# Kernel tuning notes

Hardware: AMD Instinct MI355X
Metric: run time of the kernel (lower is better)

## Reference

```python
import jax, jax.numpy as jnp
import numpy as np

N_NODES = 100000
N_EDGES = 1600000
IN_DIM = 128
HID = 128
Z_DIM = 16
NUM_LAYERS = 3


def gcn_conv(x, W, b, src, dst, num_nodes):
    """PyG-style GCNConv with self-loops and symmetric normalization.
    src/dst already include self-loops. x: [N, Fin], W: [Fin, Fout]."""
    xw = x @ W  # [N, Fout]
    deg = jax.ops.segment_sum(jnp.ones(src.shape[0], dtype=x.dtype), dst,
                              num_segments=num_nodes)  # >=1 due to self-loops
    dinv = jax.lax.rsqrt(jnp.maximum(deg, 1.0))
    norm = dinv[src] * dinv[dst]  # [E]
    msg = xw[src] * norm[:, None]  # [E, Fout] gather
    out = jax.ops.segment_sum(msg, dst, num_segments=num_nodes)  # scatter-add
    return out + b


def setup_inputs() -> dict:
    key = jax.random.key(0)
    ks = jax.random.split(key, 10)
    adj = jax.random.randint(ks[0], (2, N_EDGES), 0, N_NODES, dtype=jnp.int32)
    X = jax.random.normal(ks[1], (N_NODES, IN_DIM), dtype=jnp.float32)
    s = 0.05
    fc1_W = jax.random.normal(ks[2], (IN_DIM, 128), dtype=jnp.float32) * s
    fc1_b = jnp.zeros((128,), dtype=jnp.float32)
    fc2_W = jax.random.normal(ks[3], (128, HID), dtype=jnp.float32) * s
    fc2_b = jnp.zeros((HID,), dtype=jnp.float32)
    gcn_W = jax.random.normal(ks[4], (NUM_LAYERS, HID, HID), dtype=jnp.float32) * s
    gcn_b = jnp.zeros((NUM_LAYERS, HID), dtype=jnp.float32)
    assign_W = jax.random.normal(ks[5], (HID, Z_DIM), dtype=jnp.float32) * s
    assign_b = jnp.zeros((Z_DIM,), dtype=jnp.float32)
    return {"adj": adj, "X": X, "fc1_W": fc1_W, "fc1_b": fc1_b,
            "fc2_W": fc2_W, "fc2_b": fc2_b, "gcn_W": gcn_W, "gcn_b": gcn_b,
            "assign_W": assign_W, "assign_b": assign_b}


def reference(adj, X, fc1_W, fc1_b, fc2_W, fc2_b, gcn_W, gcn_b, assign_W, assign_b):
    n = X.shape[0]
    loop = jnp.arange(n, dtype=adj.dtype)
    src = jnp.concatenate([adj[0], loop])  # add self-loops
    dst = jnp.concatenate([adj[1], loop])
    h = jax.nn.sigmoid(X @ fc1_W + fc1_b)
    h = jax.nn.sigmoid(h @ fc2_W + fc2_b)
    for i in range(NUM_LAYERS):
        h = gcn_conv(h, gcn_W[i], gcn_b[i], src, dst, n)
    assign = gcn_conv(h, assign_W, assign_b, src, dst, n)
    return assign
```

## Files before the change

### kernel.cpp

```cpp
#include <hip/hip_runtime.h>
#include <cstdint>
#include <cstddef>


#define SCAN_CHUNK 2048

typedef _Float16 half8 __attribute__((ext_vector_type(8)));
typedef float floatx4 __attribute__((ext_vector_type(4)));

__global__ __launch_bounds__(256) void scan_partial_k(const int* __restrict__ cnt, int N,
                                                      int* __restrict__ bsum) {
  __shared__ int red[256];
  int b = blockIdx.x, t = threadIdx.x;
  int base = b * SCAN_CHUNK + t * 8;
  int s = 0;
#pragma unroll
  for (int i = 0; i < 8; ++i) {
    int idx = base + i;
    if (idx < N) s += cnt[idx];
  }
  red[t] = s;
  __syncthreads();
  for (int off = 128; off > 0; off >>= 1) {
    if (t < off) red[t] += red[t + off];
    __syncthreads();
  }
  if (t == 0) bsum[b] = red[0];
}

__global__ __launch_bounds__(64) void scan_bsum_k(int* __restrict__ bsum, int NB) {
  int lane = threadIdx.x;
  int per = (NB + 63) >> 6;
  int beg = lane * per;
  int end = min(beg + per, NB);
  int s = 0;
  for (int i = beg; i < end; ++i) s += bsum[i];
  int ps = s;
  for (int off = 1; off < 64; off <<= 1) {
    int u = __shfl_up(ps, off, 64);
    if (lane >= off) ps += u;
  }
  int run = ps - s;
  for (int i = beg; i < end; ++i) {
    int c = bsum[i];
    bsum[i] = run;
    run += c;
  }
}

__global__ __launch_bounds__(256) void scan_apply_k(const int* __restrict__ cnt,
                                                    const int* __restrict__ bsum_excl, int N,
                                                    int* __restrict__ rowptr,
                                                    int* __restrict__ cursor, int E) {
  __shared__ int wave_sums[4];
  int b = blockIdx.x, t = threadIdx.x;
  int base = b * SCAN_CHUNK + t * 8;
  int v[8];
  int s = 0;
#pragma unroll
  for (int i = 0; i < 8; ++i) {
    int idx = base + i;
    v[i] = (idx < N) ? cnt[idx] : 0;
    s += v[i];
  }
  int lane = t & 63, wave = t >> 6;
  int ps = s;
  for (int off = 1; off < 64; off <<= 1) {
    int u = __shfl_up(ps, off, 64);
    if (lane >= off) ps += u;
  }
  if (lane == 63) wave_sums[wave] = ps;
  __syncthreads();
  int woff = 0;
  for (int w = 0; w < 4; ++w)
    if (w < wave) woff += wave_sums[w];
  int excl = woff + (ps - s) + bsum_excl[b];
#pragma unroll
  for (int i = 0; i < 8; ++i) {
    int idx = base + i;
    if (idx < N) {
      rowptr[idx] = excl;
      cursor[idx] = excl;
      excl += v[i];
    }
  }
  if (b == 0 && t == 0) rowptr[N] = E;
}

__global__ __launch_bounds__(256) void p1a_hist_k(const int* __restrict__ dst, int E, int G,
                                                  int B, int chunk, int* __restrict__ M) {
  __shared__ int h[256];
  int g = blockIdx.x, t = threadIdx.x;
  for (int i = t; i < B; i += 256) h[i] = 0;
  __syncthreads();
  int ebeg = g * chunk, eend = min(ebeg + chunk, E);
  for (int e = ebeg + t; e < eend; e += 256) atomicAdd(&h[dst[e] >> 9], 1);
  __syncthreads();
  for (int b = t; b < B; b += 256) M[(size_t)b * G + g] = h[b];
}

__global__ __launch_bounds__(256) void p1c_scatter_k(const int* __restrict__ src,
                                                     const int* __restrict__ dst, int E, int G,
                                                     int B, int chunk,
                                                     const int* __restrict__ scanned,
                                                     uint32_t* __restrict__ tmp) {
  __shared__ int off[256];
  int g = blockIdx.x, t = threadIdx.x;
  for (int b = t; b < B; b += 256) off[b] = scanned[(size_t)b * G + g];
  __syncthreads();
  int ebeg = g * chunk, eend = min(ebeg + chunk, E);
  for (int e = ebeg + t; e < eend; e += 256) {
    int d = dst[e];
    int b = d >> 9;
    int pos = atomicAdd(&off[b], 1);
    tmp[pos] = ((uint32_t)(d & 511) << 17) | (uint32_t)src[e];
  }
}

__global__ __launch_bounds__(256) void p2_build_k(const uint32_t* __restrict__ tmp,
                                                  const int* __restrict__ scanned, int G, int N,
                                                  int E, int* __restrict__ rowptr,
                                                  int* __restrict__ col,
                                                  float* __restrict__ dinv,
                                                  float* __restrict__ dinv2) {
  __shared__ int hist[512];
  __shared__ int cur[512];
  __shared__ int wsum[4];
  int b = blockIdx.x, t = threadIdx.x;
  int node0 = b << 9;
  int nn = min(512, N - node0);
  int sbeg = scanned[(size_t)b * G];
  int send = scanned[(size_t)(b + 1) * G];
  for (int i = t; i < 512; i += 256) hist[i] = 0;
  __syncthreads();
  for (int e = sbeg + t; e < send; e += 256) atomicAdd(&hist[tmp[e] >> 17], 1);
  __syncthreads();
  int h0 = hist[2 * t], h1 = hist[2 * t + 1];
  int s = h0 + h1;
  int lane = t & 63, w = t >> 6;
  int ps = s;
  for (int o = 1; o < 64; o <<= 1) {
    int u = __shfl_up(ps, o, 64);
    if (lane >= o) ps += u;
  }
  if (lane == 63) wsum[w] = ps;
  __syncthreads();
  int woff = 0;
  for (int k = 0; k < 4; ++k)
    if (k < w) woff += wsum[k];
  int excl = sbeg + woff + (ps - s);
  if (2 * t < nn) {
    rowptr[node0 + 2 * t] = excl;
    cur[2 * t] = excl;
    dinv[node0 + 2 * t] = rsqrtf((float)(h0 + 1));
    dinv2[node0 + 2 * t] = 1.f / (float)(h0 + 1);
  }
  if (2 * t + 1 < nn) {
    rowptr[node0 + 2 * t + 1] = excl + h0;
    cur[2 * t + 1] = excl + h0;
    dinv[node0 + 2 * t + 1] = rsqrtf((float)(h1 + 1));
    dinv2[node0 + 2 * t + 1] = 1.f / (float)(h1 + 1);
  }
  if (b == 0 && t == 0) rowptr[N] = E;
  __syncthreads();
  for (int e = sbeg + t; e < send; e += 256) {
    uint32_t u = tmp[e];
    int pos = atomicAdd(&cur[u >> 17], 1);
    col[pos] = (int)(u & 0x1FFFF);
  }
}

__global__ __launch_bounds__(256) void count_edges_k(const int* __restrict__ dst, int E,
                                                     int* __restrict__ cnt) {
  int idx = blockIdx.x * blockDim.x + threadIdx.x;
  int stride = gridDim.x * blockDim.x;
  for (int e = idx; e < E; e += stride) atomicAdd(&cnt[dst[e]], 1);
}

__global__ __launch_bounds__(256) void dinv_k(const int* __restrict__ cnt,
                                              float* __restrict__ dinv,
                                              float* __restrict__ dinv2, int N) {
  int i = blockIdx.x * blockDim.x + threadIdx.x;
  if (i < N) {
    dinv[i] = rsqrtf((float)(cnt[i] + 1));
    dinv2[i] = 1.f / (float)(cnt[i] + 1);
  }
}

__global__ __launch_bounds__(256) void fill_k(const int* __restrict__ src,
                                              const int* __restrict__ dst, int E,
                                              int* __restrict__ cursor, int* __restrict__ col) {
  int idx = blockIdx.x * blockDim.x + threadIdx.x;
  int stride = gridDim.x * blockDim.x;
  for (int e = idx; e < E; e += stride) {
    int d = dst[e];
    int pos = atomicAdd(&cursor[d], 1);
    col[pos] = src[e];
  }
}

__global__ __launch_bounds__(256) void wprep_k(const float* __restrict__ fc1_W,
                                               const float* __restrict__ fc2_W,
                                               _Float16* __restrict__ Wb) {
  int idx = blockIdx.x * 256 + threadIdx.x;
  if (idx < 2 * 16384) {
    int mat = idx >> 14;
    int r = idx & 16383;
    int t = r >> 11;
    int ktb = (r >> 9) & 3;
    int lane = (r >> 3) & 63;
    int j = r & 7;
    int m = lane & 15, q = lane >> 4;
    int k = ktb * 32 + q * 8 + j;
    int n = t * 16 + m;
    const float* W = (mat == 0) ? fc1_W : fc2_W;
    Wb[idx] = (_Float16)W[(size_t)k * 128 + n];
  }
}

__global__ __launch_bounds__(256) void chain_mm_k(const float* __restrict__ A,
                                                  const float* __restrict__ B,
                                                  float* __restrict__ C) {
  __shared__ float Bl[2048];
  int t = threadIdx.x;
  for (int i = t; i < 2048; i += 256) Bl[i] = B[i];
  __syncthreads();
  int idx = blockIdx.x * 256 + t;
  int row = idx >> 4, f = idx & 15;
  const float* Ar = A + (size_t)row * 128;
  float s = 0.f;
#pragma unroll 8
  for (int j = 0; j < 128; ++j) s = fmaf(Ar[j], Bl[j * 16 + f], s);
  C[idx] = s;
}

__global__ __launch_bounds__(256) void chain_frag_k(const float* __restrict__ W0,
                                                    const float* __restrict__ T1,
                                                    const float* __restrict__ T2,
                                                    const float* __restrict__ assign_W,
                                                    const float* __restrict__ gcn_b,
                                                    _Float16* __restrict__ WbT,
                                                    float* __restrict__ cvec) {
  int t = threadIdx.x;
  if (blockIdx.x < 8) {
    __shared__ float T1l[2048];
    for (int i = t; i < 2048; i += 256) T1l[i] = T1[i];
    __syncthreads();
    int idx = blockIdx.x * 256 + t;
    int ktb = idx >> 9;
    int lane = (idx >> 3) & 63;
    int jj = idx & 7;
    int m = lane & 15, qq = lane >> 4;
    int k = ktb * 32 + qq * 8 + jj;
    const float* Ar = W0 + (size_t)k * 128;
    float s = 0.f;
#pragma unroll 8
    for (int j = 0; j < 128; ++j) s = fmaf(Ar[j], T1l[j * 16 + m], s);
    WbT[idx] = (_Float16)s;
  } else {
    if (t < 16) {
      float s3 = 0.f, s2 = 0.f, s1 = 0.f;
      for (int k = 0; k < 128; ++k) {
        s3 += gcn_b[k] * T1[k * 16 + t];
        s2 += gcn_b[128 + k] * T2[k * 16 + t];
        s1 += gcn_b[256 + k] * assign_W[k * 16 + t];
      }
      cvec[t] = s3;
      cvec[16 + t] = s2;
      cvec[32 + t] = s1;
    }
  }
}

__global__ __launch_bounds__(256) void mlp_fused_k(const float* __restrict__ X,
                                                   const _Float16* __restrict__ Wb,
                                                   const float* __restrict__ fc1_b,
                                                   const float* __restrict__ fc2_b,
                                                   const _Float16* __restrict__ WbT,
                                                   const float* __restrict__ dinv,
                                                   _Float16* __restrict__ S, int N) {
  __shared__ _Float16 Wst[16384];
  __shared__ _Float16 hl[4][16 * 136];
  const int tid = threadIdx.x;
  const int w = tid >> 6, lane = tid & 63;
  const int m = lane & 15, q = lane >> 4;
  const int r0 = (blockIdx.x * 4 + w) * 16;
  const int rowA = r0 + m;
  const bool validA = rowA < N;
  _Float16* hw = hl[w];

  float4 xa[8];
#pragma unroll
  for (int ktb = 0; ktb < 4; ++ktb) {
    if (validA) {
      const float* Ap = X + (size_t)rowA * 128 + ktb * 32 + q * 8;
      xa[2 * ktb] = *(const float4*)Ap;
      xa[2 * ktb + 1] = *(const float4*)(Ap + 4);
    } else {
      xa[2 * ktb] = (float4){0.f, 0.f, 0.f, 0.f};
      xa[2 * ktb + 1] = (float4){0.f, 0.f, 0.f, 0.f};
    }
  }
  {
    half8 v[8];
#pragma unroll
    for (int i = 0; i < 8; ++i) v[i] = *(const half8*)(Wb + ((size_t)(i * 256 + tid)) * 8);
#pragma unroll
    for (int i = 0; i < 8; ++i) *(half8*)(Wst + (size_t)(i * 256 + tid) * 8) = v[i];
  }
  __syncthreads();

  floatx4 acc[8];
#pragma unroll
  for (int t = 0; t < 8; ++t) acc[t] = (floatx4){0.f, 0.f, 0.f, 0.f};
#pragma unroll
  for (int ktb = 0; ktb < 4; ++ktb) {
    half8 a;
    float4 f0 = xa[2 * ktb], f1 = xa[2 * ktb + 1];
    a[0] = (_Float16)f0.x; a[1] = (_Float16)f0.y;
    a[2] = (_Float16)f0.z; a[3] = (_Float16)f0.w;
    a[4] = (_Float16)f1.x; a[5] = (_Float16)f1.y;
    a[6] = (_Float16)f1.z; a[7] = (_Float16)f1.w;
#pragma unroll
    for (int t = 0; t < 8; ++t) {
      half8 b = *(const half8*)(Wst + ((size_t)(t * 4 + ktb) * 64 + lane) * 8);
      acc[t] = __builtin_amdgcn_mfma_f32_16x16x32_f16(a, b, acc[t], 0, 0, 0);
    }
  }
#pragma unroll
  for (int t = 0; t < 8; ++t) {
    int colg = t * 16 + m;
    float bz = fc1_b[colg];
#pragma unroll
    for (int r = 0; r < 4; ++r) {
      float v = acc[t][r] + bz;
      v = 1.f / (1.f + __expf(-v));
      hw[(q * 4 + r) * 136 + colg] = (_Float16)v;
    }
  }
  __syncthreads();
  {
    const _Float16* Wb2 = Wb + 16384;
    half8 v[8];
#pragma unroll
    for (int i = 0; i < 8; ++i) v[i] = *(const half8*)(Wb2 + ((size_t)(i * 256 + tid)) * 8);
#pragma unroll
    for (int i = 0; i < 8; ++i) *(half8*)(Wst + (size_t)(i * 256 + tid) * 8) = v[i];
  }
  __syncthreads();

#pragma unroll
  for (int t = 0; t < 8; ++t) acc[t] = (floatx4){0.f, 0.f, 0.f, 0.f};
#pragma unroll
  for (int ktb = 0; ktb < 4; ++ktb) {
    half8 a = *(const half8*)(hw + m * 136 + ktb * 32 + q * 8);
#pragma unroll
    for (int t = 0; t < 8; ++t) {
      half8 b = *(const half8*)(Wst + ((size_t)(t * 4 + ktb) * 64 + lane) * 8);
      acc[t] = __builtin_amdgcn_mfma_f32_16x16x32_f16(a, b, acc[t], 0, 0, 0);
    }
  }
#pragma unroll
  for (int t = 0; t < 8; ++t) {
    int colg = t * 16 + m;
    float bz = fc2_b[colg];
#pragma unroll
    for (int r = 0; r < 4; ++r) {
      float v = acc[t][r] + bz;
      v = 1.f / (1.f + __expf(-v));
      hw[(q * 4 + r) * 136 + colg] = (_Float16)v;
    }
  }
  floatx4 p0 = (floatx4){0.f, 0.f, 0.f, 0.f};
#pragma unroll
  for (int ktb = 0; ktb < 4; ++ktb) {
    half8 a = *(const half8*)(hw + m * 136 + ktb * 32 + q * 8);
    half8 b = *(const half8*)(WbT + ((size_t)ktb * 64 + lane) * 8);
    p0 = __builtin_amdgcn_mfma_f32_16x16x32_f16(a, b, p0, 0, 0, 0);
  }
#pragma unroll
  for (int r = 0; r < 4; ++r) {
    int row = r0 + q * 4 + r;
    if (row < N) S[(size_t)row * 16 + m] = (_Float16)(p0[r] * dinv[row]);
  }
}

template <bool FOUT32>
__global__ __launch_bounds__(256) void agg16h_k(const _Float16* __restrict__ xw,
                                                const int* __restrict__ rowptr,
                                                const int* __restrict__ col,
                                                const float* __restrict__ rowscale,
                                                const float* __restrict__ biasmul,
                                                const float* __restrict__ c,
                                                void* __restrict__ outv, int N) {
  int node = blockIdx.x * 4 + (threadIdx.x >> 6);
  if (node >= N) return;
  int lane = threadIdx.x & 63;
  int f = lane & 15;
  int j = lane >> 4;
  int beg = rowptr[node];
  int end = rowptr[node + 1];
  int deg = end - beg;
  int q = (deg + 3) >> 2;
  int e = beg + j * q;
  int e1 = min(e + q, end);
  float acc = 0.f;
  for (; e + 3 < e1; e += 4) {
    int s0 = col[e], s1 = col[e + 1], s2 = col[e + 2], s3 = col[e + 3];
    float v0 = (float)xw[(size_t)s0 * 16 + f];
    float v1 = (float)xw[(size_t)s1 * 16 + f];
    float v2 = (float)xw[(size_t)s2 * 16 + f];
    float v3 = (float)xw[(size_t)s3 * 16 + f];
    acc += (v0 + v1) + (v2 + v3);
  }
  for (; e < e1; ++e) acc += (float)xw[(size_t)col[e] * 16 + f];
  acc += __shfl_xor(acc, 16, 64);
  acc += __shfl_xor(acc, 32, 64);
  if (j == 0) {
    acc += (float)xw[(size_t)node * 16 + f];
    float bm = biasmul ? biasmul[node] : 1.f;
    float o = fmaf(acc, rowscale[node], bm * c[f]);
    if (FOUT32)
      ((float*)outv)[(size_t)node * 16 + f] = o;
    else
      ((_Float16*)outv)[(size_t)node * 16 + f] = (_Float16)o;
  }
}

extern "C" void kernel_launch(void* const* d_in, const int* in_sizes, int n_in,
                              void* d_out, int out_size, void* d_ws, size_t ws_size,
                              hipStream_t stream) {
  const int* adj = (const int*)d_in[0];
  const float* X = (const float*)d_in[1];
  const float* fc1_W = (const float*)d_in[2];
  const float* fc1_b = (const float*)d_in[3];
  const float* fc2_W = (const float*)d_in[4];
  const float* fc2_b = (const float*)d_in[5];
  const float* gcn_W = (const float*)d_in[6];
  const float* gcn_b = (const float*)d_in[7];
  const float* assign_W = (const float*)d_in[8];
  const float* assign_b = (const float*)d_in[9];
  const int E = in_sizes[0] / 2;
  const int N = in_sizes[1] / 128;
  const int* src = adj;
  const int* dst = adj + E;

  char* ws = (char*)d_ws;
  size_t off = 0;
  auto alloc = [&](size_t bytes) {
    void* p = ws + off;
    off = (off + bytes + 511) & ~(size_t)511;
    return p;
  };
  const int G = 256;
  const int B = (N + 511) >> 9;
  const int L = B * G;
  _Float16* SA = (_Float16*)alloc((size_t)N * 16 * 2);
  _Float16* SB = (_Float16*)alloc((size_t)N * 16 * 2);
  _Float16* Wb = (_Float16*)alloc((size_t)2 * 16384 * 2);
  _Float16* WbT = (_Float16*)alloc(2048 * 2);
  float* T2g = (float*)alloc(2048 * 4);
  float* T1g = (float*)alloc(2048 * 4);
  float* cvec = (float*)alloc(48 * 4);
  float* dinv = (float*)alloc((size_t)N * 4);
  float* dinv2 = (float*)alloc((size_t)N * 4);
  int* rowptr = (int*)alloc((size_t)(N + 1) * 4);
  int* col = (int*)alloc((size_t)E * 4);
  uint32_t* tmp = (uint32_t*)alloc((size_t)E * 4);
  int* M = (int*)alloc((size_t)L * 4);
  int* scanned = (int*)alloc((size_t)(L + 1) * 4);
  int* scanscratch = (int*)alloc((size_t)L * 4);
  int* bsum = (int*)alloc(4096);
  int* cnt = (int*)alloc((size_t)N * 4);
  int* cursor = (int*)alloc((size_t)N * 4);

  wprep_k<<<(2 * 16384 + 255) / 256, 256, 0, stream>>>(fc1_W, fc2_W, Wb);
  chain_mm_k<<<8, 256, 0, stream>>>(gcn_W + 32768, assign_W, T2g);
  chain_mm_k<<<8, 256, 0, stream>>>(gcn_W + 16384, T2g, T1g);
  chain_frag_k<<<9, 256, 0, stream>>>(gcn_W, T1g, T2g, assign_W, gcn_b, WbT, cvec);

  if (N <= (1 << 17)) {
    const int chunk = (E + G - 1) / G;
    const int NBL = (L + SCAN_CHUNK - 1) / SCAN_CHUNK;
    p1a_hist_k<<<G, 256, 0, stream>>>(dst, E, G, B, chunk, M);
    scan_partial_k<<<NBL, 256, 0, stream>>>(M, L, bsum);
    scan_bsum_k<<<1, 64, 0, stream>>>(bsum, NBL);
    scan_apply_k<<<NBL, 256, 0, stream>>>(M, bsum, L, scanned, scanscratch, E);
    p1c_scatter_k<<<G, 256, 0, stream>>>(src, dst, E, G, B, chunk, scanned, tmp);
    p2_build_k<<<B, 256, 0, stream>>>(tmp, scanned, G, N, E, rowptr, col, dinv, dinv2);
  } else {
    const int NB = (N + SCAN_CHUNK - 1) / SCAN_CHUNK;
    hipMemsetAsync(cnt, 0, (size_t)N * 4, stream);
    count_edges_k<<<2048, 256, 0, stream>>>(dst, E, cnt);
    dinv_k<<<(N + 255) / 256, 256, 0, stream>>>(cnt, dinv, dinv2, N);
    scan_partial_k<<<NB, 256, 0, stream>>>(cnt, N, bsum);
    scan_bsum_k<<<1, 64, 0, stream>>>(bsum, NB);
    scan_apply_k<<<NB, 256, 0, stream>>>(cnt, bsum, N, rowptr, cursor, E);
    fill_k<<<2048, 256, 0, stream>>>(src, dst, E, cursor, col);
  }

  int gfuse = (N + 63) / 64;
  int ab = (N + 3) / 4;
  mlp_fused_k<<<gfuse, 256, 0, stream>>>(X, Wb, fc1_b, fc2_b, WbT, dinv, SA, N);
  agg16h_k<false><<<ab, 256, 0, stream>>>(SA, rowptr, col, dinv2, dinv, cvec, SB, N);
  agg16h_k<false><<<ab, 256, 0, stream>>>(SB, rowptr, col, dinv2, dinv, cvec + 16, SA, N);
  agg16h_k<false><<<ab, 256, 0, stream>>>(SA, rowptr, col, dinv2, dinv, cvec + 32, SB, N);
  agg16h_k<true><<<ab, 256, 0, stream>>>(SB, rowptr, col, dinv, nullptr, assign_b,
                                         (float*)d_out, N);
}
```

Measured before the change: 365.8 us.

## Aggregate directly from bucketed edge list with shared-memory atomics, drop CSR build

Shrinks the destination buckets from 512 to 128 nodes (G raised to 1024) and stops building a full CSR. The bucketed packed edge array is consumed directly by a new aggregation kernel: one block per bucket accumulates 16-wide fp16 neighbour rows into an LDS tile with float atomics. This removes the second per-bucket sort pass and the col/rowptr writes. It adds many LDS atomic adds per edge, changes the summation order, and enlarges the histogram and scan arrays.

```diff
diff --git a/kernel.cpp b/kernel.cpp
--- a/kernel.cpp
+++ b/kernel.cpp
@@ -89,12 +89,12 @@
 
 __global__ __launch_bounds__(256) void p1a_hist_k(const int* __restrict__ dst, int E, int G,
                                                   int B, int chunk, int* __restrict__ M) {
-  __shared__ int h[256];
+  __shared__ int h[1024];
   int g = blockIdx.x, t = threadIdx.x;
   for (int i = t; i < B; i += 256) h[i] = 0;
   __syncthreads();
   int ebeg = g * chunk, eend = min(ebeg + chunk, E);
-  for (int e = ebeg + t; e < eend; e += 256) atomicAdd(&h[dst[e] >> 9], 1);
+  for (int e = ebeg + t; e < eend; e += 256) atomicAdd(&h[dst[e] >> 7], 1);
   __syncthreads();
   for (int b = t; b < B; b += 256) M[(size_t)b * G + g] = h[b];
 }
@@ -104,69 +104,38 @@
                                                      int B, int chunk,
                                                      const int* __restrict__ scanned,
                                                      uint32_t* __restrict__ tmp) {
-  __shared__ int off[256];
+  __shared__ int off[1024];
   int g = blockIdx.x, t = threadIdx.x;
   for (int b = t; b < B; b += 256) off[b] = scanned[(size_t)b * G + g];
   __syncthreads();
   int ebeg = g * chunk, eend = min(ebeg + chunk, E);
   for (int e = ebeg + t; e < eend; e += 256) {
     int d = dst[e];
-    int b = d >> 9;
+    int b = d >> 7;
     int pos = atomicAdd(&off[b], 1);
-    tmp[pos] = ((uint32_t)(d & 511) << 17) | (uint32_t)src[e];
-  }
-}
-
-__global__ __launch_bounds__(256) void p2_build_k(const uint32_t* __restrict__ tmp,
-                                                  const int* __restrict__ scanned, int G, int N,
-                                                  int E, int* __restrict__ rowptr,
-                                                  int* __restrict__ col,
-                                                  float* __restrict__ dinv,
-                                                  float* __restrict__ dinv2) {
-  __shared__ int hist[512];
-  __shared__ int cur[512];
-  __shared__ int wsum[4];
+    tmp[pos] = ((uint32_t)(d & 127) << 17) | (uint32_t)src[e];
+  }
+}
+
+__global__ __launch_bounds__(256) void p2v2_k(const uint32_t* __restrict__ tmp,
+                                              const int* __restrict__ scanned, int G, int N,
+                                              float* __restrict__ dinv,
+                                              float* __restrict__ dinv2) {
+  __shared__ int hist[128];
   int b = blockIdx.x, t = threadIdx.x;
-  int node0 = b << 9;
-  int nn = min(512, N - node0);
+  if (t < 128) hist[t] = 0;
+  __syncthreads();
   int sbeg = scanned[(size_t)b * G];
   int send = scanned[(size_t)(b + 1) * G];
-  for (int i = t; i < 512; i += 256) hist[i] = 0;
-  __syncthreads();
   for (int e = sbeg + t; e < send; e += 256) atomicAdd(&hist[tmp[e] >> 17], 1);
   __syncthreads();
-  int h0 = hist[2 * t], h1 = hist[2 * t + 1];
-  int s = h0 + h1;
-  int lane = t & 63, w = t >> 6;
-  int ps = s;
-  for (int o = 1; o < 64; o <<= 1) {
-    int u = __shfl_up(ps, o, 64);
-    if (lane >= o) ps += u;
-  }
-  if (lane == 63) wsum[w] = ps;
-  __syncthreads();
-  int woff = 0;
-  for (int k = 0; k < 4; ++k)
-    if (k < w) woff += wsum[k];
-  int excl = sbeg + woff + (ps - s);
-  if (2 * t < nn) {
-    rowptr[node0 + 2 * t] = excl;
-    cur[2 * t] = excl;
-    dinv[node0 + 2 * t] = rsqrtf((float)(h0 + 1));
-    dinv2[node0 + 2 * t] = 1.f / (float)(h0 + 1);
-  }
-  if (2 * t + 1 < nn) {
-    rowptr[node0 + 2 * t + 1] = excl + h0;
-    cur[2 * t + 1] = excl + h0;
-    dinv[node0 + 2 * t + 1] = rsqrtf((float)(h1 + 1));
-    dinv2[node0 + 2 * t + 1] = 1.f / (float)(h1 + 1);
-  }
-  if (b == 0 && t == 0) rowptr[N] = E;
-  __syncthreads();
-  for (int e = sbeg + t; e < send; e += 256) {
-    uint32_t u = tmp[e];
-    int pos = atomicAdd(&cur[u >> 17], 1);
-    col[pos] = (int)(u & 0x1FFFF);
+  if (t < 128) {
+    int node = (b << 7) + t;
+    if (node < N) {
+      float d = (float)(hist[t] + 1);
+      dinv[node] = rsqrtf(d);
+      dinv2[node] = 1.f / d;
+    }
   }
 }
 
@@ -386,6 +355,96 @@
 }
 
 template <bool FOUT32>
+__global__ __launch_bounds__(256) void agg16v3_k(const _Float16* __restrict__ xw,
+                                                 const uint32_t* __restrict__ tmp,
+                                                 const int* __restrict__ scanned, int G,
+                                                 const float* __restrict__ rowscale,
+                                                 const float* __restrict__ biasmul,
+                                                 const float* __restrict__ c,
+                                                 void* __restrict__ outv, int N) {
+  __shared__ float acc[128][17];
+  int b = blockIdx.x, tid = threadIdx.x;
+  int node0 = b << 7;
+  if (tid < 128) {
+    int node = node0 + tid;
+    if (node < N) {
+      const _Float16* sp = xw + (size_t)node * 16;
+      half8 lo = *(const half8*)sp;
+      half8 hi = *(const half8*)(sp + 8);
+#pragma unroll
+      for (int f = 0; f < 8; ++f) {
+        acc[tid][f] = (float)lo[f];
+        acc[tid][8 + f] = (float)hi[f];
+      }
+    } else {
+#pragma unroll
+      for (int f = 0; f < 16; ++f) acc[tid][f] = 0.f;
+    }
+  }
+  __syncthreads();
+  int sbeg = scanned[(size_t)b * G];
+  int send = scanned[(size_t)(b + 1) * G];
+  int e = sbeg + tid;
+  for (; e + 768 < send; e += 1024) {
+    uint32_t u0 = tmp[e], u1 = tmp[e + 256], u2 = tmp[e + 512], u3 = tmp[e + 768];
+    int r0 = u0 >> 17, r1 = u1 >> 17, r2 = u2 >> 17, r3 = u3 >> 17;
+    const _Float16* p0 = xw + (size_t)(u0 & 0x1FFFF) * 16;
+    const _Float16* p1 = xw + (size_t)(u1 & 0x1FFFF) * 16;
+    const _Float16* p2 = xw + (size_t)(u2 & 0x1FFFF) * 16;
+    const _Float16* p3 = xw + (size_t)(u3 & 0x1FFFF) * 16;
+    half8 lo0 = *(const half8*)p0, hi0 = *(const half8*)(p0 + 8);
+    half8 lo1 = *(const half8*)p1, hi1 = *(const half8*)(p1 + 8);
+    half8 lo2 = *(const half8*)p2, hi2 = *(const half8*)(p2 + 8);
+    half8 lo3 = *(const half8*)p3, hi3 = *(const half8*)(p3 + 8);
+#pragma unroll
+    for (int f = 0; f < 8; ++f) {
+      atomicAdd(&acc[r0][f], (float)lo0[f]);
+      atomicAdd(&acc[r0][8 + f], (float)hi0[f]);
+      atomicAdd(&acc[r1][f], (float)lo1[f]);
+      atomicAdd(&acc[r1][8 + f], (float)hi1[f]);
+      atomicAdd(&acc[r2][f], (float)lo2[f]);
+      atomicAdd(&acc[r2][8 + f], (float)hi2[f]);
+      atomicAdd(&acc[r3][f], (float)lo3[f]);
+      atomicAdd(&acc[r3][8 + f], (float)hi3[f]);
+    }
+  }
+  for (; e < send; e += 256) {
+    uint32_t u = tmp[e];
+    int r = u >> 17;
+    const _Float16* p = xw + (size_t)(u & 0x1FFFF) * 16;
+    half8 lo = *(const half8*)p, hi = *(const half8*)(p + 8);
+#pragma unroll
+    for (int f = 0; f < 8; ++f) {
+      atomicAdd(&acc[r][f], (float)lo[f]);
+      atomicAdd(&acc[r][8 + f], (float)hi[f]);
+    }
+  }
+  __syncthreads();
+  if (tid < 128) {
+    int node = node0 + tid;
+    if (node < N) {
+      float rs = rowscale[node];
+      float bm = biasmul ? biasmul[node] : 1.f;
+      if (FOUT32) {
+        float* op = (float*)outv + (size_t)node * 16;
+#pragma unroll
+        for (int f = 0; f < 16; ++f) op[f] = fmaf(acc[tid][f], rs, bm * c[f]);
+      } else {
+        half8 o0, o1;
+#pragma unroll
+        for (int f = 0; f < 8; ++f) {
+          o0[f] = (_Float16)fmaf(acc[tid][f], rs, bm * c[f]);
+          o1[f] = (_Float16)fmaf(acc[tid][8 + f], rs, bm * c[8 + f]);
+        }
+        _Float16* op = (_Float16*)outv + (size_t)node * 16;
+        *(half8*)op = o0;
+        *(half8*)(op + 8) = o1;
+      }
+    }
+  }
+}
+
+template <bool FOUT32>
 __global__ __launch_bounds__(256) void agg16h_k(const _Float16* __restrict__ xw,
                                                 const int* __restrict__ rowptr,
                                                 const int* __restrict__ col,
@@ -406,11 +465,10 @@
   int e1 = min(e + q, end);
   float acc = 0.f;
   for (; e + 3 < e1; e += 4) {
-    int s0 = col[e], s1 = col[e + 1], s2 = col[e + 2], s3 = col[e + 3];
-    float v0 = (float)xw[(size_t)s0 * 16 + f];
-    float v1 = (float)xw[(size_t)s1 * 16 + f];
-    float v2 = (float)xw[(size_t)s2 * 16 + f];
-    float v3 = (float)xw[(size_t)s3 * 16 + f];
+    float v0 = (float)xw[(size_t)col[e] * 16 + f];
+    float v1 = (float)xw[(size_t)col[e + 1] * 16 + f];
+    float v2 = (float)xw[(size_t)col[e + 2] * 16 + f];
+    float v3 = (float)xw[(size_t)col[e + 3] * 16 + f];
     acc += (v0 + v1) + (v2 + v3);
   }
   for (; e < e1; ++e) acc += (float)xw[(size_t)col[e] * 16 + f];
@@ -452,8 +510,8 @@
     off = (off + bytes + 511) & ~(size_t)511;
     return p;
   };
-  const int G = 256;
-  const int B = (N + 511) >> 9;
+  const int G = 1024;
+  const int B = (N + 127) >> 7;
   const int L = B * G;
   _Float16* SA = (_Float16*)alloc((size_t)N * 16 * 2);
   _Float16* SB = (_Float16*)alloc((size_t)N * 16 * 2);
@@ -479,6 +537,7 @@
   chain_mm_k<<<8, 256, 0, stream>>>(gcn_W + 16384, T2g, T1g);
   chain_frag_k<<<9, 256, 0, stream>>>(gcn_W, T1g, T2g, assign_W, gcn_b, WbT, cvec);
 
+  int gfuse = (N + 63) / 64;
   if (N <= (1 << 17)) {
     const int chunk = (E + G - 1) / G;
     const int NBL = (L + SCAN_CHUNK - 1) / SCAN_CHUNK;
@@ -487,7 +546,14 @@
     scan_bsum_k<<<1, 64, 0, stream>>>(bsum, NBL);
     scan_apply_k<<<NBL, 256, 0, stream>>>(M, bsum, L, scanned, scanscratch, E);
     p1c_scatter_k<<<G, 256, 0, stream>>>(src, dst, E, G, B, chunk, scanned, tmp);
-    p2_build_k<<<B, 256, 0, stream>>>(tmp, scanned, G, N, E, rowptr, col, dinv, dinv2);
+    p2v2_k<<<B, 256, 0, stream>>>(tmp, scanned, G, N, dinv, dinv2);
+
+    mlp_fused_k<<<gfuse, 256, 0, stream>>>(X, Wb, fc1_b, fc2_b, WbT, dinv, SA, N);
+    agg16v3_k<false><<<B, 256, 0, stream>>>(SA, tmp, scanned, G, dinv2, dinv, cvec, SB, N);
+    agg16v3_k<false><<<B, 256, 0, stream>>>(SB, tmp, scanned, G, dinv2, dinv, cvec + 16, SA, N);
+    agg16v3_k<false><<<B, 256, 0, stream>>>(SA, tmp, scanned, G, dinv2, dinv, cvec + 32, SB, N);
+    agg16v3_k<true><<<B, 256, 0, stream>>>(SB, tmp, scanned, G, dinv, nullptr, assign_b,
+                                           (float*)d_out, N);
   } else {
     const int NB = (N + SCAN_CHUNK - 1) / SCAN_CHUNK;
     hipMemsetAsync(cnt, 0, (size_t)N * 4, stream);
@@ -497,14 +563,13 @@
     scan_bsum_k<<<1, 64, 0, stream>>>(bsum, NB);
     scan_apply_k<<<NB, 256, 0, stream>>>(cnt, bsum, N, rowptr, cursor, E);
     fill_k<<<2048, 256, 0, stream>>>(src, dst, E, cursor, col);
-  }
-
-  int gfuse = (N + 63) / 64;
-  int ab = (N + 3) / 4;
-  mlp_fused_k<<<gfuse, 256, 0, stream>>>(X, Wb, fc1_b, fc2_b, WbT, dinv, SA, N);
-  agg16h_k<false><<<ab, 256, 0, stream>>>(SA, rowptr, col, dinv2, dinv, cvec, SB, N);
-  agg16h_k<false><<<ab, 256, 0, stream>>>(SB, rowptr, col, dinv2, dinv, cvec + 16, SA, N);
-  agg16h_k<false><<<ab, 256, 0, stream>>>(SA, rowptr, col, dinv2, dinv, cvec + 32, SB, N);
-  agg16h_k<true><<<ab, 256, 0, stream>>>(SB, rowptr, col, dinv, nullptr, assign_b,
-                                         (float*)d_out, N);
-}
+
+    int ab = (N + 3) / 4;
+    mlp_fused_k<<<gfuse, 256, 0, stream>>>(X, Wb, fc1_b, fc2_b, WbT, dinv, SA, N);
+    agg16h_k<false><<<ab, 256, 0, stream>>>(SA, rowptr, col, dinv2, dinv, cvec, SB, N);
+    agg16h_k<false><<<ab, 256, 0, stream>>>(SB, rowptr, col, dinv2, dinv, cvec + 16, SA, N);
+    agg16h_k<false><<<ab, 256, 0, stream>>>(SA, rowptr, col, dinv2, dinv, cvec + 32, SB, N);
+    agg16h_k<true><<<ab, 256, 0, stream>>>(SB, rowptr, col, dinv, nullptr, assign_b,
+                                           (float*)d_out, N);
+  }
+}
```

Result: slower. 903.0 us (+146.8%).

## Aggregate four nodes per wavefront with merged edge ranges and prefix partial sums

Applied to the files above, without the earlier changes.

The 16-wide aggregation kernel now gives each wavefront four consecutive nodes instead of one. Their contiguous CSR edge range is split evenly across the four 16-lane groups, and each group keeps four running sums masked by node boundaries. After a cross-group reduction, each node's value is taken as the difference of adjacent sums. The aim is to balance load across the low-degree rows (about 17 edges each) and raise memory-level parallelism with an 8-wide unrolled gather, at the cost of extra compares, adds and shuffles. Taking differences of float sums can also lose a little precision.

```diff
diff --git a/kernel.cpp b/kernel.cpp
--- a/kernel.cpp
+++ b/kernel.cpp
@@ -386,44 +386,71 @@
 }
 
 template <bool FOUT32>
-__global__ __launch_bounds__(256) void agg16h_k(const _Float16* __restrict__ xw,
+__global__ __launch_bounds__(256) void agg16q_k(const _Float16* __restrict__ xw,
                                                 const int* __restrict__ rowptr,
                                                 const int* __restrict__ col,
                                                 const float* __restrict__ rowscale,
                                                 const float* __restrict__ biasmul,
                                                 const float* __restrict__ c,
                                                 void* __restrict__ outv, int N) {
-  int node = blockIdx.x * 4 + (threadIdx.x >> 6);
-  if (node >= N) return;
+  int w = blockIdx.x * 4 + (threadIdx.x >> 6);
+  int n0 = w * 4;
+  if (n0 >= N) return;
   int lane = threadIdx.x & 63;
   int f = lane & 15;
   int j = lane >> 4;
-  int beg = rowptr[node];
-  int end = rowptr[node + 1];
-  int deg = end - beg;
-  int q = (deg + 3) >> 2;
-  int e = beg + j * q;
-  int e1 = min(e + q, end);
-  float acc = 0.f;
-  for (; e + 3 < e1; e += 4) {
-    int s0 = col[e], s1 = col[e + 1], s2 = col[e + 2], s3 = col[e + 3];
-    float v0 = (float)xw[(size_t)s0 * 16 + f];
-    float v1 = (float)xw[(size_t)s1 * 16 + f];
-    float v2 = (float)xw[(size_t)s2 * 16 + f];
-    float v3 = (float)xw[(size_t)s3 * 16 + f];
-    acc += (v0 + v1) + (v2 + v3);
-  }
-  for (; e < e1; ++e) acc += (float)xw[(size_t)col[e] * 16 + f];
-  acc += __shfl_xor(acc, 16, 64);
-  acc += __shfl_xor(acc, 32, 64);
-  if (j == 0) {
-    acc += (float)xw[(size_t)node * 16 + f];
-    float bm = biasmul ? biasmul[node] : 1.f;
-    float o = fmaf(acc, rowscale[node], bm * c[f]);
+  int b0 = rowptr[n0];
+  int s1 = rowptr[min(n0 + 1, N)];
+  int s2 = rowptr[min(n0 + 2, N)];
+  int s3 = rowptr[min(n0 + 3, N)];
+  int e4 = rowptr[min(n0 + 4, N)];
+  int D = e4 - b0;
+  int q = (D + 3) >> 2;
+  int e = b0 + j * q;
+  int ee = min(e + q, e4);
+  float p0 = 0.f, p1 = 0.f, p2 = 0.f, p3 = 0.f;
+  for (; e + 7 < ee; e += 8) {
+    int cc[8];
+#pragma unroll
+    for (int i = 0; i < 8; ++i) cc[i] = col[e + i];
+    float vv[8];
+#pragma unroll
+    for (int i = 0; i < 8; ++i) vv[i] = (float)xw[(size_t)cc[i] * 16 + f];
+#pragma unroll
+    for (int i = 0; i < 8; ++i) {
+      int ei = e + i;
+      float v = vv[i];
+      p0 += (ei < s1) ? v : 0.f;
+      p1 += (ei < s2) ? v : 0.f;
+      p2 += (ei < s3) ? v : 0.f;
+      p3 += v;
+    }
+  }
+  for (; e < ee; ++e) {
+    float v = (float)xw[(size_t)col[e] * 16 + f];
+    p0 += (e < s1) ? v : 0.f;
+    p1 += (e < s2) ? v : 0.f;
+    p2 += (e < s3) ? v : 0.f;
+    p3 += v;
+  }
+  p0 += __shfl_xor(p0, 16, 64);
+  p0 += __shfl_xor(p0, 32, 64);
+  p1 += __shfl_xor(p1, 16, 64);
+  p1 += __shfl_xor(p1, 32, 64);
+  p2 += __shfl_xor(p2, 16, 64);
+  p2 += __shfl_xor(p2, 32, 64);
+  p3 += __shfl_xor(p3, 16, 64);
+  p3 += __shfl_xor(p3, 32, 64);
+  float mine = (j == 0) ? p0 : (j == 1) ? (p1 - p0) : (j == 2) ? (p2 - p1) : (p3 - p2);
+  int nj = n0 + j;
+  if (nj < N) {
+    float a = mine + (float)xw[(size_t)nj * 16 + f];
+    float bm = biasmul ? biasmul[nj] : 1.f;
+    float o = fmaf(a, rowscale[nj], bm * c[f]);
     if (FOUT32)
-      ((float*)outv)[(size_t)node * 16 + f] = o;
+      ((float*)outv)[(size_t)nj * 16 + f] = o;
     else
-      ((_Float16*)outv)[(size_t)node * 16 + f] = (_Float16)o;
+      ((_Float16*)outv)[(size_t)nj * 16 + f] = (_Float16)o;
   }
 }
 
@@ -500,11 +527,11 @@
   }
 
   int gfuse = (N + 63) / 64;
-  int ab = (N + 3) / 4;
+  int ab = (N + 15) / 16;
   mlp_fused_k<<<gfuse, 256, 0, stream>>>(X, Wb, fc1_b, fc2_b, WbT, dinv, SA, N);
-  agg16h_k<false><<<ab, 256, 0, stream>>>(SA, rowptr, col, dinv2, dinv, cvec, SB, N);
-  agg16h_k<false><<<ab, 256, 0, stream>>>(SB, rowptr, col, dinv2, dinv, cvec + 16, SA, N);
-  agg16h_k<false><<<ab, 256, 0, stream>>>(SA, rowptr, col, dinv2, dinv, cvec + 32, SB, N);
-  agg16h_k<true><<<ab, 256, 0, stream>>>(SB, rowptr, col, dinv, nullptr, assign_b,
+  agg16q_k<false><<<ab, 256, 0, stream>>>(SA, rowptr, col, dinv2, dinv, cvec, SB, N);
+  agg16q_k<false><<<ab, 256, 0, stream>>>(SB, rowptr, col, dinv2, dinv, cvec + 16, SA, N);
+  agg16q_k<false><<<ab, 256, 0, stream>>>(SA, rowptr, col, dinv2, dinv, cvec + 32, SB, N);
+  agg16q_k<true><<<ab, 256, 0, stream>>>(SB, rowptr, col, dinv, nullptr, assign_b,
                                          (float*)d_out, N);
 }
```

Result: faster. 304.2 us (-16.8%).
